# Kernel tuning notes

Measured on AMD Instinct MI355X. Metric: run time of the kernel, lower is better.

## Reference

```python
import jax, jax.numpy as jnp
import numpy as np

B, S, T, HD = 8, 2048, 512, 4096  # batch, max_seq, update_len, n_heads*head_dim


def setup_inputs() -> dict:
    key = jax.random.key(0)
    k1, k2 = jax.random.split(key)
    return {
        "k_cache": jnp.zeros((B, S, HD), dtype=jnp.float32),
        "v_cache": jnp.zeros((B, S, HD), dtype=jnp.float32),
        "k_val": jax.random.normal(k1, (B, T, HD), dtype=jnp.float32),
        "v_val": jax.random.normal(k2, (B, T, HD), dtype=jnp.float32),
        "input_pos": jnp.arange(T, dtype=jnp.int64 if jax.config.jax_enable_x64 else jnp.int32),
    }


def reference(k_cache, v_cache, k_val, v_val, input_pos):
    # Functional equivalent of: k_cache[:, input_pos] = k_val; v_cache[:, input_pos] = v_val
    k_out = k_cache.at[:, input_pos].set(k_val)
    v_out = v_cache.at[:, input_pos].set(v_val)
    return (k_out, v_out)
```

## Files before the change

### kernel.cpp

```cpp
#include <hip/hip_runtime.h>

#define B_DIM 8
#define S_DIM 2048
#define T_DIM 512
#define HDV   1024

typedef float floatx4 __attribute__((ext_vector_type(4)));

__global__ void __launch_bounds__(256)
kv_update_kernel(const floatx4* __restrict__ k_cache,
                 const floatx4* __restrict__ v_cache,
                 const floatx4* __restrict__ k_val,
                 const floatx4* __restrict__ v_val,
                 const int* __restrict__ input_pos,
                 floatx4* __restrict__ out) {
    const unsigned per_tensor = (unsigned)B_DIM * S_DIM * HDV;
    unsigned e = blockIdx.x * blockDim.x + threadIdx.x;

    unsigned col = e & (HDV - 1);
    unsigned s   = (e >> 10) & (S_DIM - 1);
    unsigned b   = e >> 21;

    int lane = threadIdx.x & 63;
    int t = -1;
#pragma unroll
    for (int i = 0; i < T_DIM / 64; ++i) {
        int p = input_pos[i * 64 + lane];
        unsigned long long m = __ballot(p == (int)s);
        if (m) t = i * 64 + (__ffsll((long long)m) - 1);
    }

    floatx4 rk, rv;
    if (t >= 0) {
        unsigned vi = (b * (unsigned)T_DIM + (unsigned)t) * HDV + col;
        rk = __builtin_nontemporal_load(k_val + vi);
        rv = __builtin_nontemporal_load(v_val + vi);
    } else {
        rk = __builtin_nontemporal_load(k_cache + e);
        rv = __builtin_nontemporal_load(v_cache + e);
    }
    __builtin_nontemporal_store(rk, out + e);
    __builtin_nontemporal_store(rv, out + per_tensor + e);
}

extern "C" void kernel_launch(void* const* d_in, const int* in_sizes, int n_in,
                              void* d_out, int out_size, void* d_ws, size_t ws_size,
                              hipStream_t stream) {
    const floatx4* k_cache   = (const floatx4*)d_in[0];
    const floatx4* v_cache   = (const floatx4*)d_in[1];
    const floatx4* k_val     = (const floatx4*)d_in[2];
    const floatx4* v_val     = (const floatx4*)d_in[3];
    const int*     input_pos = (const int*)d_in[4];
    floatx4* out = (floatx4*)d_out;

    const unsigned per_tensor = (unsigned)B_DIM * S_DIM * HDV;
    kv_update_kernel<<<per_tensor / 256, 256, 0, stream>>>(
        k_cache, v_cache, k_val, v_val, input_pos, out);
}
```

Before: 859.8 us.

## Assign one block per cache row with four loads per thread

Each block now handles a whole (batch, seq) row of 1024 float4s instead of a quarter row. Every thread issues four K and four V nontemporal loads before its stores. The position search over input_pos runs once per row instead of four times, which cuts redundant index scanning and raises memory-level parallelism. The duplicate-position pick also switches from the first match to the last match, which is a semantic change for repeated positions.

```diff
diff --git a/kernel.cpp b/kernel.cpp
--- a/kernel.cpp
+++ b/kernel.cpp
@@ -15,11 +15,10 @@
                  const int* __restrict__ input_pos,
                  floatx4* __restrict__ out) {
     const unsigned per_tensor = (unsigned)B_DIM * S_DIM * HDV;
-    unsigned e = blockIdx.x * blockDim.x + threadIdx.x;
 
-    unsigned col = e & (HDV - 1);
-    unsigned s   = (e >> 10) & (S_DIM - 1);
-    unsigned b   = e >> 21;
+    unsigned r = blockIdx.x;
+    unsigned s = r & (S_DIM - 1);
+    unsigned b = r >> 11;
 
     int lane = threadIdx.x & 63;
     int t = -1;
@@ -27,20 +26,39 @@
     for (int i = 0; i < T_DIM / 64; ++i) {
         int p = input_pos[i * 64 + lane];
         unsigned long long m = __ballot(p == (int)s);
-        if (m) t = i * 64 + (__ffsll((long long)m) - 1);
+        if (m) t = i * 64 + (63 - __clzll((long long)m));
     }
 
-    floatx4 rk, rv;
+    const floatx4* __restrict__ srcK;
+    const floatx4* __restrict__ srcV;
+    unsigned sbase;
     if (t >= 0) {
-        unsigned vi = (b * (unsigned)T_DIM + (unsigned)t) * HDV + col;
-        rk = __builtin_nontemporal_load(k_val + vi);
-        rv = __builtin_nontemporal_load(v_val + vi);
+        sbase = (b * (unsigned)T_DIM + (unsigned)t) * HDV;
+        srcK = k_val;  srcV = v_val;
     } else {
-        rk = __builtin_nontemporal_load(k_cache + e);
-        rv = __builtin_nontemporal_load(v_cache + e);
+        sbase = (b * (unsigned)S_DIM + s) * HDV;
+        srcK = k_cache; srcV = v_cache;
     }
-    __builtin_nontemporal_store(rk, out + e);
-    __builtin_nontemporal_store(rv, out + per_tensor + e);
+    unsigned obase = (b * (unsigned)S_DIM + s) * HDV + threadIdx.x;
+    sbase += threadIdx.x;
+
+    floatx4 k0 = __builtin_nontemporal_load(srcK + sbase + 0 * 256);
+    floatx4 k1 = __builtin_nontemporal_load(srcK + sbase + 1 * 256);
+    floatx4 k2 = __builtin_nontemporal_load(srcK + sbase + 2 * 256);
+    floatx4 k3 = __builtin_nontemporal_load(srcK + sbase + 3 * 256);
+    floatx4 v0 = __builtin_nontemporal_load(srcV + sbase + 0 * 256);
+    floatx4 v1 = __builtin_nontemporal_load(srcV + sbase + 1 * 256);
+    floatx4 v2 = __builtin_nontemporal_load(srcV + sbase + 2 * 256);
+    floatx4 v3 = __builtin_nontemporal_load(srcV + sbase + 3 * 256);
+
+    __builtin_nontemporal_store(k0, out + obase + 0 * 256);
+    __builtin_nontemporal_store(k1, out + obase + 1 * 256);
+    __builtin_nontemporal_store(k2, out + obase + 2 * 256);
+    __builtin_nontemporal_store(k3, out + obase + 3 * 256);
+    __builtin_nontemporal_store(v0, out + per_tensor + obase + 0 * 256);
+    __builtin_nontemporal_store(v1, out + per_tensor + obase + 1 * 256);
+    __builtin_nontemporal_store(v2, out + per_tensor + obase + 2 * 256);
+    __builtin_nontemporal_store(v3, out + per_tensor + obase + 3 * 256);
 }
 
 extern "C" void kernel_launch(void* const* d_in, const int* in_sizes, int n_in,
@@ -53,7 +71,6 @@
     const int*     input_pos = (const int*)d_in[4];
     floatx4* out = (floatx4*)d_out;
 
-    const unsigned per_tensor = (unsigned)B_DIM * S_DIM * HDV;
-    kv_update_kernel<<<per_tensor / 256, 256, 0, stream>>>(
+    kv_update_kernel<<<B_DIM * S_DIM, 256, 0, stream>>>(
         k_cache, v_cache, k_val, v_val, input_pos, out);
 }
```

Measured after the change: 857.5 us. About the same (-0.3%).
